# Optimization experiments

Measured on AMD Instinct MI355X. Metric: run time of the kernel, lower is better.

The kernel has to match this reference:

```python
import jax, jax.numpy as jnp
import numpy as np

EMBED_DIM = 1024
NUM_HEADS = 16
HEAD_DIM = EMBED_DIM // NUM_HEADS
MAX_DIST = 128
NUM_BUCKETS = 2 * MAX_DIST + 1  # 257: fixes off-by-one in original Embedding sizing


def setup_inputs() -> dict:
    key = jax.random.key(0)
    ks = jax.random.split(key, 10)
    B, S, D = 2, 2048, EMBED_DIM
    s = 1.0 / np.sqrt(D)
    return {
        "x": jax.random.normal(ks[0], (B, S, D), dtype=jnp.float32),
        "Wq": jax.random.normal(ks[1], (D, D), dtype=jnp.float32) * s,
        "bq": jnp.zeros((D,), dtype=jnp.float32),
        "Wk": jax.random.normal(ks[2], (D, D), dtype=jnp.float32) * s,
        "bk": jnp.zeros((D,), dtype=jnp.float32),
        "Wv": jax.random.normal(ks[3], (D, D), dtype=jnp.float32) * s,
        "bv": jnp.zeros((D,), dtype=jnp.float32),
        "Wo": jax.random.normal(ks[4], (D, D), dtype=jnp.float32) * s,
        "bo": jnp.zeros((D,), dtype=jnp.float32),
        "rel_emb": jax.random.normal(ks[5], (NUM_BUCKETS, NUM_HEADS), dtype=jnp.float32) * 0.02,
    }


def _rel_bias(rel_emb, seq_len):
    # relative position clamped to [-MAX_DIST, MAX_DIST], shifted to [0, 2*MAX_DIST]
    pos = jnp.arange(seq_len)
    rel = jnp.clip(pos[:, None] - pos[None, :], -MAX_DIST, MAX_DIST) + MAX_DIST
    bias = rel_emb[rel]                    # [S, S, H]
    return jnp.transpose(bias, (2, 0, 1))  # [H, S, S]


def reference(x, Wq, bq, Wk, bk, Wv, bv, Wo, bo, rel_emb):
    B, S, D = x.shape
    H, Hd = NUM_HEADS, HEAD_DIM
    # torch Linear: y = x @ W.T + b
    q = (x @ Wq.T + bq).reshape(B, S, H, Hd).transpose(0, 2, 1, 3)  # [B,H,S,Hd]
    k = (x @ Wk.T + bk).reshape(B, S, H, Hd).transpose(0, 2, 1, 3)
    v = (x @ Wv.T + bv).reshape(B, S, H, Hd).transpose(0, 2, 1, 3)
    scores = jnp.einsum("bhqd,bhkd->bhqk", q, k) / jnp.sqrt(jnp.float32(Hd))
    scores = scores + _rel_bias(rel_emb, S)[None]  # add [H,S,S] bias
    probs = jax.nn.softmax(scores, axis=-1)
    out = jnp.einsum("bhqk,bhkd->bhqd", probs, v)
    out = out.transpose(0, 2, 1, 3).reshape(B, S, D)
    return out @ Wo.T + bo
```

## Files before the change

### kernel.cpp

```cpp
#include <hip/hip_runtime.h>
#include <hip/hip_bf16.h>
#include <cstdint>
#include <cstddef>

#define DEVI __device__ __forceinline__

static constexpr int SEQ = 2048;
static constexpr int DM  = 1024;
static constexpr int NH  = 16;
static constexpr int HD  = 64;
static constexpr int NTOK = 2 * SEQ;
static constexpr int NBUCKET = 257;
static constexpr float LOG2E = 1.44269504088896f;

typedef __attribute__((ext_vector_type(8))) short bf16x8;
typedef __attribute__((ext_vector_type(4))) float f32x4;
typedef __attribute__((ext_vector_type(16))) float f32x16;
typedef __attribute__((ext_vector_type(2))) unsigned int uint32x2;
#define MFMA16(a, b, c) __builtin_amdgcn_mfma_f32_16x16x32_bf16((a), (b), (c), 0, 0, 0)
#define MFMA32(a, b, c) __builtin_amdgcn_mfma_f32_32x32x16_bf16((a), (b), (c), 0, 0, 0)

DEVI float bf1(uint16_t u)  { return __uint_as_float(((uint32_t)u) << 16); }
DEVI uint16_t f2bf(float f) {
    uint32_t x = __float_as_uint(f);
    x += 0x7fffu + ((x >> 16) & 1u);
    return (uint16_t)(x >> 16);
}
DEVI bf16x8 ld_frag(const uint16_t* p) {
    union { uint4 u; bf16x8 f; } c;
    c.u = *(const uint4*)p;
    return c.f;
}
DEVI void gld16(const uint16_t* g, uint16_t* l) {
    __builtin_amdgcn_global_load_lds(
        (const __attribute__((address_space(1))) uint32_t*)g,
        (__attribute__((address_space(3))) uint32_t*)l, 16, 0, 0);
}
DEVI uint32_t cvt_pk_bf16(float lo, float hi) {
    uint32_t r;
    asm("v_cvt_pk_bf16_f32 %0, %1, %2" : "=v"(r) : "v"(lo), "v"(hi));
    return r;
}
DEVI void pl32(uint32_t &a, uint32_t &b) {
    const uint32x2 r = __builtin_amdgcn_permlane32_swap(a, b, false, false);
    a = r[0]; b = r[1];
}

__global__ void sniff_kernel(const uint16_t* __restrict__ x, int* __restrict__ flag)
{
    int bad = 0;
    for (int i = threadIdx.x; i < 512; i += 64) {
        const float v = bf1(x[i]);
        if (!(fabsf(v) < 64.0f)) bad = 1;
    }
    const unsigned long long m = __ballot(bad);
    if (threadIdx.x == 0) *flag = (m != 0ull) ? 1 : 0;
}

__global__ __launch_bounds__(256)
void convert_kernel(const void* __restrict__ x, const void* __restrict__ Wq,
                    const void* __restrict__ Wk, const void* __restrict__ Wv,
                    const void* __restrict__ Wo, const void* __restrict__ bq,
                    const void* __restrict__ bk, const void* __restrict__ bv,
                    const void* __restrict__ bo, uint16_t* __restrict__ dst,
                    const int* __restrict__ flagp)
{
    const bool f32in = (*flagp != 0);
    const size_t M4 = 4194304, M1 = 1048576;
    const size_t e = ((size_t)blockIdx.x * 256 + threadIdx.x) * 8;
    const void* src; size_t off;
    if      (e < M4)                 { src = x;  off = e; }
    else if (e < M4 + M1)            { src = Wq; off = e - M4; }
    else if (e < M4 + 2*M1)          { src = Wk; off = e - M4 - M1; }
    else if (e < M4 + 3*M1)          { src = Wv; off = e - M4 - 2*M1; }
    else if (e < M4 + 4*M1)          { src = Wo; off = e - M4 - 3*M1; }
    else if (e < M4 + 4*M1 + 1024)   { src = bq; off = e - M4 - 4*M1; }
    else if (e < M4 + 4*M1 + 2048)   { src = bk; off = e - M4 - 4*M1 - 1024; }
    else if (e < M4 + 4*M1 + 3072)   { src = bv; off = e - M4 - 4*M1 - 2048; }
    else                             { src = bo; off = e - M4 - 4*M1 - 3072; }
    if (f32in) {
        const float4 a = *(const float4*)((const float*)src + off);
        const float4 b = *(const float4*)((const float*)src + off + 4);
        uint4 o;
        o.x = (uint32_t)f2bf(a.x) | ((uint32_t)f2bf(a.y) << 16);
        o.y = (uint32_t)f2bf(a.z) | ((uint32_t)f2bf(a.w) << 16);
        o.z = (uint32_t)f2bf(b.x) | ((uint32_t)f2bf(b.y) << 16);
        o.w = (uint32_t)f2bf(b.z) | ((uint32_t)f2bf(b.w) << 16);
        *(uint4*)(dst + e) = o;
    } else {
        *(uint4*)(dst + e) = *(const uint4*)((const uint16_t*)src + off);
    }
}

__global__ __launch_bounds__(256)
void gemm_qkv(const uint16_t* __restrict__ xc, const uint16_t* __restrict__ Wqkv,
              const uint16_t* __restrict__ bqkv,
              uint16_t* __restrict__ Qw, uint16_t* __restrict__ Kw,
              uint16_t* __restrict__ Vt)
{
    __shared__ uint16_t As[128 * 32];
    __shared__ uint16_t Bs[128 * 32];
    const int tid = threadIdx.x, bx = blockIdx.x;
    const int lane = tid & 63, wave = tid >> 6;
    const int ln = lane & 15, quad = lane >> 4;
    const int wm = (wave & 1) * 64, wn = (wave >> 1) * 64;

    const uint16_t *Ab, *Bb;
    int bm, bn, vor;
    if (bx < 512) {
        vor = 0; bm = (bx >> 4) * 128; bn = (bx & 15) * 128;
        Ab = xc + (size_t)bm * DM;  Bb = Wqkv + (size_t)bn * DM;
    } else {
        vor = 1; const int b2 = bx - 512; bm = (b2 >> 5) * 128; bn = (b2 & 31) * 128;
        Ab = Wqkv + (size_t)(2048 + bm) * DM;  Bb = xc + (size_t)bn * DM;
    }

    f32x4 acc[4][4];
    #pragma unroll
    for (int i = 0; i < 4; ++i)
        #pragma unroll
        for (int j = 0; j < 4; ++j) acc[i][j] = (f32x4){0.f, 0.f, 0.f, 0.f};

    const int s0 = tid, s1 = 256 + tid;
    const uint16_t* ga0 = Ab + (size_t)(s0 >> 2) * DM + (s0 & 3) * 8;
    const uint16_t* ga1 = Ab + (size_t)(s1 >> 2) * DM + (s1 & 3) * 8;
    const uint16_t* gb0 = Bb + (size_t)(s0 >> 2) * DM + (s0 & 3) * 8;
    const uint16_t* gb1 = Bb + (size_t)(s1 >> 2) * DM + (s1 & 3) * 8;

    for (int k0 = 0; k0 < DM; k0 += 32) {
        __syncthreads();
        gld16(ga0 + k0, &As[s0 * 8]);
        gld16(ga1 + k0, &As[s1 * 8]);
        gld16(gb0 + k0, &Bs[s0 * 8]);
        gld16(gb1 + k0, &Bs[s1 * 8]);
        __syncthreads();

        bf16x8 af[4], bfr[4];
        #pragma unroll
        for (int t = 0; t < 4; ++t) {
            af[t]  = ld_frag(&As[(wm + t * 16 + ln) * 32 + quad * 8]);
            bfr[t] = ld_frag(&Bs[(wn + t * 16 + ln) * 32 + quad * 8]);
        }
        #pragma unroll
        for (int ti = 0; ti < 4; ++ti)
            #pragma unroll
            for (int tj = 0; tj < 4; ++tj)
                acc[ti][tj] = MFMA16(af[ti], bfr[tj], acc[ti][tj]);
    }

    if (!vor) {
        #pragma unroll
        for (int tj = 0; tj < 4; ++tj) {
            const int c = bn + wn + tj * 16 + ln;
            const int mat = c >> 10, h = (c >> 6) & 15, hd = c & 63;
            uint16_t* dstp = mat ? Kw : Qw;
            const float scale = mat ? 1.0f : (0.125f * LOG2E);
            const float bb = bf1(bqkv[c]);
            #pragma unroll
            for (int ti = 0; ti < 4; ++ti)
                #pragma unroll
                for (int r = 0; r < 4; ++r) {
                    const int row = bm + wm + ti * 16 + quad * 4 + r;
                    const int b = row >> 11, s = row & 2047;
                    dstp[(((size_t)b * NH + h) * SEQ + s) * HD + hd] =
                        f2bf((acc[ti][tj][r] + bb) * scale);
                }
        }
    } else {
        #pragma unroll
        for (int ti = 0; ti < 4; ++ti)
            #pragma unroll
            for (int r = 0; r < 4; ++r) {
                const int f = bm + wm + ti * 16 + quad * 4 + r;
                const int h = f >> 6, hd = f & 63;
                const float bb = bf1(bqkv[2048 + f]);
                #pragma unroll
                for (int tj = 0; tj < 4; ++tj) {
                    const int t = bn + wn + tj * 16 + ln;
                    const int b = t >> 11, s = t & 2047;
                    Vt[(((size_t)b * NH + h) * HD + hd) * SEQ + s] = f2bf(acc[ti][tj][r] + bb);
                }
            }
    }
}

__global__ __launch_bounds__(256)
void gemm_out(const uint16_t* __restrict__ Cw, const uint16_t* __restrict__ Woc,
              const uint16_t* __restrict__ boc, void* __restrict__ out,
              const int* __restrict__ flagp)
{
    __shared__ uint16_t As[128 * 32];
    __shared__ uint16_t Bs[64 * 32];
    const int tid = threadIdx.x, bx = blockIdx.x;
    const int lane = tid & 63, wave = tid >> 6;
    const int ln = lane & 15, quad = lane >> 4;
    const int wm = (wave & 1) * 64, wn = (wave >> 1) * 32;
    const int bm = (bx >> 4) * 128, bn = (bx & 15) * 64;
    const uint16_t* Ab = Cw + (size_t)bm * DM;
    const uint16_t* Bb = Woc + (size_t)bn * DM;

    f32x4 acc[4][2];
    #pragma unroll
    for (int i = 0; i < 4; ++i)
        #pragma unroll
        for (int j = 0; j < 2; ++j) acc[i][j] = (f32x4){0.f, 0.f, 0.f, 0.f};

    const int s0 = tid, s1 = 256 + tid;
    const uint16_t* ga0 = Ab + (size_t)(s0 >> 2) * DM + (s0 & 3) * 8;
    const uint16_t* ga1 = Ab + (size_t)(s1 >> 2) * DM + (s1 & 3) * 8;
    const uint16_t* gb0 = Bb + (size_t)(s0 >> 2) * DM + (s0 & 3) * 8;

    for (int k0 = 0; k0 < DM; k0 += 32) {
        __syncthreads();
        gld16(ga0 + k0, &As[s0 * 8]);
        gld16(ga1 + k0, &As[s1 * 8]);
        gld16(gb0 + k0, &Bs[s0 * 8]);
        __syncthreads();

        bf16x8 af[4], bfr[2];
        #pragma unroll
        for (int t = 0; t < 4; ++t)
            af[t] = ld_frag(&As[(wm + t * 16 + ln) * 32 + quad * 8]);
        #pragma unroll
        for (int t = 0; t < 2; ++t)
            bfr[t] = ld_frag(&Bs[(wn + t * 16 + ln) * 32 + quad * 8]);
        #pragma unroll
        for (int ti = 0; ti < 4; ++ti)
            #pragma unroll
            for (int tj = 0; tj < 2; ++tj)
                acc[ti][tj] = MFMA16(af[ti], bfr[tj], acc[ti][tj]);
    }

    const bool f32o = (*flagp != 0);
    #pragma unroll
    for (int tj = 0; tj < 2; ++tj) {
        const int c = bn + wn + tj * 16 + ln;
        const float bb = bf1(boc[c]);
        #pragma unroll
        for (int ti = 0; ti < 4; ++ti)
            #pragma unroll
            for (int r = 0; r < 4; ++r) {
                const int row = bm + wm + ti * 16 + quad * 4 + r;
                const float v = acc[ti][tj][r] + bb;
                if (f32o) ((float*)out)[(size_t)row * DM + c] = v;
                else      ((uint16_t*)out)[(size_t)row * DM + c] = f2bf(v);
            }
    }
}

#define P_BUILD(SA, PA_LO, PA_HI)                                              \
  do {                                                                         \
    uint32_t c0_ = cvt_pk_bf16((SA)[0], (SA)[1]);                              \
    uint32_t c1_ = cvt_pk_bf16((SA)[2], (SA)[3]);                              \
    uint32_t c2_ = cvt_pk_bf16((SA)[4], (SA)[5]);                              \
    uint32_t c3_ = cvt_pk_bf16((SA)[6], (SA)[7]);                              \
    uint32_t c4_ = cvt_pk_bf16((SA)[8], (SA)[9]);                              \
    uint32_t c5_ = cvt_pk_bf16((SA)[10], (SA)[11]);                            \
    uint32_t c6_ = cvt_pk_bf16((SA)[12], (SA)[13]);                            \
    uint32_t c7_ = cvt_pk_bf16((SA)[14], (SA)[15]);                            \
    pl32(c0_, c2_); pl32(c1_, c3_);                                            \
    pl32(c4_, c6_); pl32(c5_, c7_);                                            \
    union { uint32_t u[4]; bf16x8 f; } lo_, hi_;                               \
    lo_.u[0] = c0_; lo_.u[1] = c1_; lo_.u[2] = c2_; lo_.u[3] = c3_;            \
    hi_.u[0] = c4_; hi_.u[1] = c5_; hi_.u[2] = c6_; hi_.u[3] = c7_;            \
    (PA_LO) = lo_.f; (PA_HI) = hi_.f;                                          \
  } while (0)

#define ATTN_COMPUTE(K0, KSB, VSB)                                             \
  do {                                                                         \
    const int mode_ = ((K0) >= q0 + 256) ? 0 : (((K0) + 192 <= q0) ? 2 : 1);   \
    bf16x8 kf_[2][4], vf_[2][4];                                               \
    _Pragma("unroll")                                                          \
    for (int kb = 0; kb < 2; ++kb)                                             \
      _Pragma("unroll")                                                        \
      for (int ds = 0; ds < 4; ++ds)                                           \
        kf_[kb][ds] = ld_frag((KSB) + kfo[kb][ds]);                            \
    _Pragma("unroll")                                                          \
    for (int db = 0; db < 2; ++db)                                             \
      _Pragma("unroll")                                                        \
      for (int kc = 0; kc < 4; ++kc)                                           \
        vf_[db][kc] = ld_frag((VSB) + vfo[db][kc]);                            \
    f32x16 sa0, sa1;                                                           \
    {                                                                          \
      const float binit_ = (mode_ == 0) ? bneg : ((mode_ == 2) ? bpos : 0.f);  \
      _Pragma("unroll")                                                        \
      for (int r = 0; r < 16; ++r) { sa0[r] = binit_; sa1[r] = binit_; }       \
    }                                                                          \
    _Pragma("unroll")                                                          \
    for (int ds = 0; ds < 4; ++ds) {                                           \
      sa0 = MFMA32(kf_[0][ds], qb[ds], sa0);                                   \
      sa1 = MFMA32(kf_[1][ds], qb[ds], sa1);                                   \
    }                                                                          \
    if (mode_ == 1) {                                                          \
      const int iq0_ = q0 + wave * 32 + l31 + 128 - (K0) - 4 * hi;             \
      _Pragma("unroll")                                                        \
      for (int r = 0; r < 16; ++r) {                                           \
        const int ko_ = (r & 3) + 8 * (r >> 2);                                \
        const int x0_ = max(0, min(256, iq0_ - ko_));                          \
        const int x1_ = max(0, min(256, iq0_ - 32 - ko_));                     \
        sa0[r] += bias_s[x0_];                                                 \
        sa1[r] += bias_s[x1_];                                                 \
      }                                                                        \
    }                                                                          \
    _Pragma("unroll")                                                          \
    for (int r = 0; r < 16; ++r) {                                             \
      sa0[r] = __builtin_amdgcn_exp2f(sa0[r]);                                 \
      sa1[r] = __builtin_amdgcn_exp2f(sa1[r]);                                 \
    }                                                                          \
    bf16x8 pa_[4];                                                             \
    P_BUILD(sa0, pa_[0], pa_[1]);                                              \
    P_BUILD(sa1, pa_[2], pa_[3]);                                              \
    _Pragma("unroll")                                                          \
    for (int kc = 0; kc < 4; ++kc) {                                           \
      lf    = MFMA32(pa_[kc], onef, lf);                                       \
      o2[0] = MFMA32(pa_[kc], vf_[0][kc], o2[0]);                              \
      o2[1] = MFMA32(pa_[kc], vf_[1][kc], o2[1]);                              \
    }                                                                          \
  } while (0)

__global__ __launch_bounds__(256, 2)
void attn_mfma(const uint16_t* __restrict__ Q, const uint16_t* __restrict__ K,
               const uint16_t* __restrict__ Vt, const void* __restrict__ rel,
               uint16_t* __restrict__ ctx, const int* __restrict__ flagp)
{
    __shared__ alignas(16) uint16_t Ks[2][64 * 64];
    __shared__ alignas(16) uint16_t Vls[2][64 * 64];
    __shared__ float bias_s[NBUCKET];

    const bool f32in = (*flagp != 0);
    const int tid = threadIdx.x, wave = tid >> 6, lane = tid & 63;
    const int l31 = lane & 31, hi = lane >> 5;

    const int blk = blockIdx.x;
    const int bh = (blk & 7) * 4 + ((blk >> 3) & 3);
    const int qt = blk >> 5;
    const int b = bh >> 4, h = bh & 15;
    const int q0 = qt * 128;

    const float C8 = 8.0f * LOG2E;
    for (int i = tid; i < NBUCKET; i += 256) {
        const float bv = f32in ? ((const float*)rel)[i * NH + h]
                               : bf1(((const uint16_t*)rel)[i * NH + h]);
        bias_s[i] = bv * LOG2E - C8;
    }

    bf16x8 qb[4];
    {
        const uint16_t* qp = Q + ((size_t)bh * SEQ + q0 + wave * 32 + l31) * HD;
        #pragma unroll
        for (int ds = 0; ds < 4; ++ds)
            qb[ds] = ld_frag(qp + ds * 16 + hi * 8);
    }

    union { uint4 u; bf16x8 f; } onec;
    onec.u = (uint4){0x3F803F80u, 0x3F803F80u, 0x3F803F80u, 0x3F803F80u};
    const bf16x8 onef = onec.f;

    f32x16 o2[2], lf;
    #pragma unroll
    for (int r = 0; r < 16; ++r) { o2[0][r] = 0.f; o2[1][r] = 0.f; lf[r] = 0.f; }

    const int s0_ = tid, s1_ = tid + 256;
    const int r0_ = s0_ >> 3, c0s_ = (s0_ & 7) ^ (r0_ & 7);
    const int r1_ = s1_ >> 3, c1s_ = (s1_ & 7) ^ (r1_ & 7);
    const int koff0 = r0_ * HD + c0s_ * 8,  koff1 = r1_ * HD + c1s_ * 8;
    const int voff0 = r0_ * SEQ + c0s_ * 8, voff1 = r1_ * SEQ + c1s_ * 8;
    uint16_t* const kd00 = &Ks[0][s0_ * 8];
    uint16_t* const kd01 = &Ks[0][s1_ * 8];
    uint16_t* const kd10 = &Ks[1][s0_ * 8];
    uint16_t* const kd11 = &Ks[1][s1_ * 8];
    uint16_t* const vd00 = &Vls[0][s0_ * 8];
    uint16_t* const vd01 = &Vls[0][s1_ * 8];
    uint16_t* const vd10 = &Vls[1][s0_ * 8];
    uint16_t* const vd11 = &Vls[1][s1_ * 8];

    const uint16_t* kg = K  + (size_t)bh * SEQ * HD;
    const uint16_t* vg = Vt + (size_t)bh * HD * SEQ;

    const int swz = l31 & 7;
    int kfo[2][4], vfo[2][4];
    #pragma unroll
    for (int kb = 0; kb < 2; ++kb)
        #pragma unroll
        for (int ds = 0; ds < 4; ++ds)
            kfo[kb][ds] = (kb * 32 + l31) * 64 + ((ds * 2 + hi) ^ swz) * 8;
    #pragma unroll
    for (int db = 0; db < 2; ++db)
        #pragma unroll
        for (int kc = 0; kc < 4; ++kc)
            vfo[db][kc] = (db * 32 + l31) * 64 + ((kc * 2 + hi) ^ swz) * 8;

    gld16(kg + koff0, kd00); gld16(kg + koff1, kd01);
    gld16(vg + voff0, vd00); gld16(vg + voff1, vd01);
    kg += 64 * HD; vg += 64;
    __syncthreads();
    const float bneg = bias_s[0], bpos = bias_s[256];

    for (int t = 0; t < 16; ++t) {
        gld16(kg + koff0, kd10); gld16(kg + koff1, kd11);
        gld16(vg + voff0, vd10); gld16(vg + voff1, vd11);
        kg += 64 * HD; vg += 64;
        ATTN_COMPUTE(t * 128, &Ks[0][0], &Vls[0][0]);
        __syncthreads();

        if (t < 15) {
            gld16(kg + koff0, kd00); gld16(kg + koff1, kd01);
            gld16(vg + voff0, vd00); gld16(vg + voff1, vd01);
            kg += 64 * HD; vg += 64;
        }
        ATTN_COMPUTE(t * 128 + 64, &Ks[1][0], &Vls[1][0]);
        __syncthreads();
    }

    #pragma unroll
    for (int r = 0; r < 16; ++r) {
        const float inv = 1.0f / lf[r];
        const int qq = q0 + wave * 32 + (r & 3) + 8 * (r >> 2) + 4 * hi;
        #pragma unroll
        for (int db = 0; db < 2; ++db)
            ctx[(((size_t)b * SEQ + qq) * NH + h) * HD + db * 32 + l31] =
                f2bf(o2[db][r] * inv);
    }
}

extern "C" void kernel_launch(void* const* d_in, const int* in_sizes, int n_in,
                              void* d_out, int out_size, void* d_ws, size_t ws_size,
                              hipStream_t stream)
{
    const void* x   = d_in[0];
    const void* Wq  = d_in[1];
    const void* bq  = d_in[2];
    const void* Wk  = d_in[3];
    const void* bk  = d_in[4];
    const void* Wv  = d_in[5];
    const void* bv  = d_in[6];
    const void* Wo  = d_in[7];
    const void* bo  = d_in[8];
    const void* rel = d_in[9];

    const size_t M4 = 4194304, M1 = 1048576;
    uint16_t* ws16 = (uint16_t*)d_ws;
    uint16_t* xc   = ws16;
    uint16_t* Wqkv = ws16 + M4;
    uint16_t* Woc  = ws16 + M4 + 3 * M1;
    uint16_t* bqkv = ws16 + M4 + 4 * M1;
    uint16_t* boc  = bqkv + 3072;
    uint16_t* Qw   = ws16 + M4 + 4 * M1 + 8192;
    uint16_t* Kw   = Qw + M4;
    uint16_t* Vt   = Kw + M4;
    int* flag = (int*)(Vt + M4);
    uint16_t* Cw = xc;

    sniff_kernel<<<1, 64, 0, stream>>>((const uint16_t*)x, flag);
    convert_kernel<<<4098, 256, 0, stream>>>(x, Wq, Wk, Wv, Wo, bq, bk, bv, bo,
                                             ws16, flag);
    gemm_qkv<<<768, 256, 0, stream>>>(xc, Wqkv, bqkv, Qw, Kw, Vt);
    attn_mfma<<<512, 256, 0, stream>>>(Qw, Kw, Vt, rel, Cw, flag);
    gemm_out<<<512, 256, 0, stream>>>(Cw, Woc, boc, d_out, flag);
}
```

Baseline: 205.3 us.

## Double-buffer LDS tiles in QKV and output projection GEMMs

Both projection GEMM kernels now use two shared-memory buffers per operand, issuing the global-to-LDS load for the next K slice before computing on the current one. This is meant to hide global load latency behind MFMA work and halve the number of barriers per K step. It doubles the LDS footprint per block, which may reduce occupancy, and its correctness depends on gld16 writes being complete by the following barrier.

Measured after the change: 207.9 us. Within noise of the previous version (+1.3%).

```diff
diff --git a/kernel.cpp b/kernel.cpp
--- a/kernel.cpp
+++ b/kernel.cpp
@@ -92,14 +92,29 @@
     }
 }
 
+#define QKV_STEP(AS, BS)                                                       \
+  do {                                                                         \
+    bf16x8 af[4], bfr[4];                                                      \
+    _Pragma("unroll")                                                          \
+    for (int t4 = 0; t4 < 4; ++t4) {                                           \
+        af[t4]  = ld_frag(&(AS)[(wm + t4 * 16 + ln) * 32 + quad * 8]);         \
+        bfr[t4] = ld_frag(&(BS)[(wn + t4 * 16 + ln) * 32 + quad * 8]);         \
+    }                                                                          \
+    _Pragma("unroll")                                                          \
+    for (int ti = 0; ti < 4; ++ti)                                             \
+      _Pragma("unroll")                                                        \
+      for (int tj = 0; tj < 4; ++tj)                                           \
+        acc[ti][tj] = MFMA16(af[ti], bfr[tj], acc[ti][tj]);                    \
+  } while (0)
+
 __global__ __launch_bounds__(256)
 void gemm_qkv(const uint16_t* __restrict__ xc, const uint16_t* __restrict__ Wqkv,
               const uint16_t* __restrict__ bqkv,
               uint16_t* __restrict__ Qw, uint16_t* __restrict__ Kw,
               uint16_t* __restrict__ Vt)
 {
-    __shared__ uint16_t As[128 * 32];
-    __shared__ uint16_t Bs[128 * 32];
+    __shared__ uint16_t As[2][128 * 32];
+    __shared__ uint16_t Bs[2][128 * 32];
     const int tid = threadIdx.x, bx = blockIdx.x;
     const int lane = tid & 63, wave = tid >> 6;
     const int ln = lane & 15, quad = lane >> 4;
@@ -127,25 +142,30 @@
     const uint16_t* gb0 = Bb + (size_t)(s0 >> 2) * DM + (s0 & 3) * 8;
     const uint16_t* gb1 = Bb + (size_t)(s1 >> 2) * DM + (s1 & 3) * 8;
 
-    for (int k0 = 0; k0 < DM; k0 += 32) {
-        __syncthreads();
-        gld16(ga0 + k0, &As[s0 * 8]);
-        gld16(ga1 + k0, &As[s1 * 8]);
-        gld16(gb0 + k0, &Bs[s0 * 8]);
-        gld16(gb1 + k0, &Bs[s1 * 8]);
-        __syncthreads();
-
-        bf16x8 af[4], bfr[4];
-        #pragma unroll
-        for (int t = 0; t < 4; ++t) {
-            af[t]  = ld_frag(&As[(wm + t * 16 + ln) * 32 + quad * 8]);
-            bfr[t] = ld_frag(&Bs[(wn + t * 16 + ln) * 32 + quad * 8]);
+    gld16(ga0, &As[0][s0 * 8]);
+    gld16(ga1, &As[0][s1 * 8]);
+    gld16(gb0, &Bs[0][s0 * 8]);
+    gld16(gb1, &Bs[0][s1 * 8]);
+    __syncthreads();
+
+    for (int t = 0; t < 16; ++t) {
+        const int kB = t * 64 + 32;
+        gld16(ga0 + kB, &As[1][s0 * 8]);
+        gld16(ga1 + kB, &As[1][s1 * 8]);
+        gld16(gb0 + kB, &Bs[1][s0 * 8]);
+        gld16(gb1 + kB, &Bs[1][s1 * 8]);
+        QKV_STEP(As[0], Bs[0]);
+        __syncthreads();
+
+        if (t < 15) {
+            const int kA = t * 64 + 64;
+            gld16(ga0 + kA, &As[0][s0 * 8]);
+            gld16(ga1 + kA, &As[0][s1 * 8]);
+            gld16(gb0 + kA, &Bs[0][s0 * 8]);
+            gld16(gb1 + kA, &Bs[0][s1 * 8]);
         }
-        #pragma unroll
-        for (int ti = 0; ti < 4; ++ti)
-            #pragma unroll
-            for (int tj = 0; tj < 4; ++tj)
-                acc[ti][tj] = MFMA16(af[ti], bfr[tj], acc[ti][tj]);
+        QKV_STEP(As[1], Bs[1]);
+        __syncthreads();
     }
 
     if (!vor) {
@@ -184,13 +204,29 @@
     }
 }
 
+#define GO_STEP(AS, BS)                                                        \
+  do {                                                                         \
+    bf16x8 af[4], bfr[2];                                                      \
+    _Pragma("unroll")                                                          \
+    for (int t4 = 0; t4 < 4; ++t4)                                             \
+        af[t4] = ld_frag(&(AS)[(wm + t4 * 16 + ln) * 32 + quad * 8]);          \
+    _Pragma("unroll")                                                          \
+    for (int t2 = 0; t2 < 2; ++t2)                                             \
+        bfr[t2] = ld_frag(&(BS)[(wn + t2 * 16 + ln) * 32 + quad * 8]);         \
+    _Pragma("unroll")                                                          \
+    for (int ti = 0; ti < 4; ++ti)                                             \
+      _Pragma("unroll")                                                        \
+      for (int tj = 0; tj < 2; ++tj)                                           \
+        acc[ti][tj] = MFMA16(af[ti], bfr[tj], acc[ti][tj]);                    \
+  } while (0)
+
 __global__ __launch_bounds__(256)
 void gemm_out(const uint16_t* __restrict__ Cw, const uint16_t* __restrict__ Woc,
               const uint16_t* __restrict__ boc, void* __restrict__ out,
               const int* __restrict__ flagp)
 {
-    __shared__ uint16_t As[128 * 32];
-    __shared__ uint16_t Bs[64 * 32];
+    __shared__ uint16_t As[2][128 * 32];
+    __shared__ uint16_t Bs[2][64 * 32];
     const int tid = threadIdx.x, bx = blockIdx.x;
     const int lane = tid & 63, wave = tid >> 6;
     const int ln = lane & 15, quad = lane >> 4;
@@ -210,25 +246,27 @@
     const uint16_t* ga1 = Ab + (size_t)(s1 >> 2) * DM + (s1 & 3) * 8;
     const uint16_t* gb0 = Bb + (size_t)(s0 >> 2) * DM + (s0 & 3) * 8;
 
-    for (int k0 = 0; k0 < DM; k0 += 32) {
-        __syncthreads();
-        gld16(ga0 + k0, &As[s0 * 8]);
-        gld16(ga1 + k0, &As[s1 * 8]);
-        gld16(gb0 + k0, &Bs[s0 * 8]);
-        __syncthreads();
-
-        bf16x8 af[4], bfr[2];
-        #pragma unroll
-        for (int t = 0; t < 4; ++t)
-            af[t] = ld_frag(&As[(wm + t * 16 + ln) * 32 + quad * 8]);
-        #pragma unroll
-        for (int t = 0; t < 2; ++t)
-            bfr[t] = ld_frag(&Bs[(wn + t * 16 + ln) * 32 + quad * 8]);
-        #pragma unroll
-        for (int ti = 0; ti < 4; ++ti)
-            #pragma unroll
-            for (int tj = 0; tj < 2; ++tj)
-                acc[ti][tj] = MFMA16(af[ti], bfr[tj], acc[ti][tj]);
+    gld16(ga0, &As[0][s0 * 8]);
+    gld16(ga1, &As[0][s1 * 8]);
+    gld16(gb0, &Bs[0][s0 * 8]);
+    __syncthreads();
+
+    for (int t = 0; t < 16; ++t) {
+        const int kB = t * 64 + 32;
+        gld16(ga0 + kB, &As[1][s0 * 8]);
+        gld16(ga1 + kB, &As[1][s1 * 8]);
+        gld16(gb0 + kB, &Bs[1][s0 * 8]);
+        GO_STEP(As[0], Bs[0]);
+        __syncthreads();
+
+        if (t < 15) {
+            const int kA = t * 64 + 64;
+            gld16(ga0 + kA, &As[0][s0 * 8]);
+            gld16(ga1 + kA, &As[0][s1 * 8]);
+            gld16(gb0 + kA, &Bs[0][s0 * 8]);
+        }
+        GO_STEP(As[1], Bs[1]);
+        __syncthreads();
     }
 
     const bool f32o = (*flagp != 0);
```
